# Kernel tuning notes

Measured on AMD Instinct MI355X. Metric: run time of the kernel, lower is better.

## Reference

```python
import jax, jax.numpy as jnp
import numpy as np

TIME_STEP = 32
BATCH = 1048576


def setup_inputs() -> dict:
    key = jax.random.key(0)
    k_x, k_w, k_b = jax.random.split(key, 3)
    inputs = jax.random.normal(k_x, (BATCH, TIME_STEP), dtype=jnp.float32)
    # Row t of W holds the weights of nn.Linear(t+1, 1); entries j>t are unused (masked).
    # Match torch Linear init scale: U(-1/sqrt(fan_in), 1/sqrt(fan_in)) per row, roughly -> just use small uniform.
    W = jax.random.uniform(k_w, (TIME_STEP, TIME_STEP), dtype=jnp.float32, minval=-0.5, maxval=0.5)
    b = jax.random.uniform(k_b, (TIME_STEP,), dtype=jnp.float32, minval=-0.5, maxval=0.5)
    return {"inputs": inputs, "W": W, "b": b}


def reference(inputs, W, b):
    # out[n, t] = sum_{j <= t} W[t, j] * inputs[n, j] + b[t]
    # Fuse the T tiny linears into one triangular-masked matmul.
    Wtri = jnp.tril(W)                       # [T, T] lower triangular
    return jnp.einsum("nj,tj->nt", inputs, Wtri) + b  # [B, T]
```

## Files before the change

### kernel.cpp

```cpp
#include <hip/hip_runtime.h>


constexpr int T    = 32;
constexpr int ROWS = 256;

__global__ __launch_bounds__(256) void triu_kernel(
    const float* __restrict__ x, const float* __restrict__ W,
    const float* __restrict__ b, float* __restrict__ out)
{
    __shared__ float4 sX[ROWS * 8];

    const int tid  = threadIdx.x;
    const int lane = tid & 63;
    const int wid  = tid >> 6;
    const long long base4 = (long long)blockIdx.x * (ROWS * 8);

    const float4* __restrict__ x4 = reinterpret_cast<const float4*>(x) + base4;

    #pragma unroll
    for (int it = 0; it < 8; ++it) {
        const int s   = it * 256 + wid * 64 + lane;
        const int row = s >> 3;
        const int c   = (s & 7) ^ (row & 7);
        __builtin_amdgcn_global_load_lds(
            (const __attribute__((address_space(1))) void*)(x4 + row * 8 + c),
            (__attribute__((address_space(3))) void*)(&sX[it * 256 + wid * 64]),
            16, 0, 0);
    }
    __syncthreads();

    const int r7 = tid & 7;
    float xr[T];
    #pragma unroll
    for (int k = 0; k < 8; ++k) {
        const float4 v = sX[tid * 8 + (k ^ r7)];
        xr[4 * k + 0] = v.x; xr[4 * k + 1] = v.y;
        xr[4 * k + 2] = v.z; xr[4 * k + 3] = v.w;
    }

    float acc[T];
    #pragma unroll
    for (int t = 0; t < T; ++t) {
        float a = b[t];
        #pragma unroll
        for (int j = 0; j <= t; ++j)
            a = fmaf(W[t * T + j], xr[j], a);
        acc[t] = a;
    }

    #pragma unroll
    for (int k = 0; k < 8; ++k)
        sX[tid * 8 + (k ^ r7)] = make_float4(acc[4 * k + 0], acc[4 * k + 1],
                                             acc[4 * k + 2], acc[4 * k + 3]);
    __syncthreads();

    float4* __restrict__ o4 = reinterpret_cast<float4*>(out) + base4;
    #pragma unroll
    for (int it = 0; it < 8; ++it) {
        const int idx = it * 256 + tid;
        const int row = idx >> 3;
        o4[idx] = sX[row * 8 + ((idx & 7) ^ (row & 7))];
    }
}

extern "C" void kernel_launch(void* const* d_in, const int* in_sizes, int n_in,
                              void* d_out, int out_size, void* d_ws, size_t ws_size,
                              hipStream_t stream) {
    const float* x  = (const float*)d_in[0];
    const float* W  = (const float*)d_in[1];
    const float* b  = (const float*)d_in[2];
    float* out      = (float*)d_out;

    const int batch = in_sizes[0] / T;
    const int grid  = batch / ROWS;
    triu_kernel<<<grid, 256, 0, stream>>>(x, W, b, out);
}
```

Baseline: 243.5 us.

## Make blocks persistent over several tiles with double-buffered async LDS loads

Each block now handles eight 256-row tiles instead of one. While the current tile is computed and stored, the next tile is prefetched into a second LDS buffer with global_load_lds. Manual vmcnt/lgkmcnt waits and s_barrier calls sequence the buffers, and the grid shrinks by the tile factor. This aims to hide load latency and cut launch/block overhead. In exchange, doubling LDS per block with a grid of only a few blocks per CU lowers occupancy and memory-level parallelism.

```diff
diff --git a/kernel.cpp b/kernel.cpp
--- a/kernel.cpp
+++ b/kernel.cpp
@@ -1,66 +1,88 @@
 #include <hip/hip_runtime.h>
 
 
-constexpr int T    = 32;
-constexpr int ROWS = 256;
+constexpr int T         = 32;
+constexpr int ROWS      = 256;
+constexpr int TPB_TILES = 8;
 
 __global__ __launch_bounds__(256) void triu_kernel(
     const float* __restrict__ x, const float* __restrict__ W,
     const float* __restrict__ b, float* __restrict__ out)
 {
-    __shared__ float4 sX[ROWS * 8];
+    __shared__ float4 sX[2][ROWS * 8];
 
     const int tid  = threadIdx.x;
     const int lane = tid & 63;
     const int wid  = tid >> 6;
-    const long long base4 = (long long)blockIdx.x * (ROWS * 8);
+    const int r7   = tid & 7;
 
-    const float4* __restrict__ x4 = reinterpret_cast<const float4*>(x) + base4;
+    const float4* __restrict__ x4 = reinterpret_cast<const float4*>(x);
+    float4*       __restrict__ o4 = reinterpret_cast<float4*>(out);
 
-    #pragma unroll
-    for (int it = 0; it < 8; ++it) {
-        const int s   = it * 256 + wid * 64 + lane;
-        const int row = s >> 3;
-        const int c   = (s & 7) ^ (row & 7);
-        __builtin_amdgcn_global_load_lds(
-            (const __attribute__((address_space(1))) void*)(x4 + row * 8 + c),
-            (__attribute__((address_space(3))) void*)(&sX[it * 256 + wid * 64]),
-            16, 0, 0);
+    const long long tile0 = (long long)blockIdx.x * TPB_TILES;
+
+    const int lrow = lane >> 3;
+    const int lsrc = wid * 64 + lrow * 8 + ((lane & 7) ^ lrow);
+
+    #define STAGE(g, buf)                                                     \
+        do {                                                                  \
+            const float4* _src = x4 + (tile0 + (g)) * (ROWS * 8) + lsrc;      \
+            _Pragma("unroll")                                                 \
+            for (int it = 0; it < 8; ++it) {                                  \
+                __builtin_amdgcn_global_load_lds(                             \
+                    (const __attribute__((address_space(1))) void*)(_src + it * 256), \
+                    (__attribute__((address_space(3))) void*)(&sX[(buf)][it * 256 + wid * 64]), \
+                    16, 0, 0);                                                \
+            }                                                                 \
+        } while (0)
+
+    STAGE(0, 0);
+
+    for (int i = 0; i < TPB_TILES; ++i) {
+        const int cur = i & 1;
+
+        if (i == 0) { asm volatile("s_waitcnt vmcnt(0)" ::: "memory"); }
+        else        { asm volatile("s_waitcnt vmcnt(8)" ::: "memory"); }
+        __builtin_amdgcn_sched_barrier(0);
+        __builtin_amdgcn_s_barrier();
+
+        if (i + 1 < TPB_TILES) STAGE(i + 1, cur ^ 1);
+
+        float xr[T];
+        #pragma unroll
+        for (int k = 0; k < 8; ++k) {
+            const float4 v = sX[cur][tid * 8 + (k ^ r7)];
+            xr[4*k+0] = v.x; xr[4*k+1] = v.y; xr[4*k+2] = v.z; xr[4*k+3] = v.w;
+        }
+
+        float acc[T];
+        #pragma unroll
+        for (int t = 0; t < T; ++t) {
+            float a = b[t];
+            #pragma unroll
+            for (int j = 0; j <= t; ++j)
+                a = fmaf(W[t * T + j], xr[j], a);
+            acc[t] = a;
+        }
+
+        #pragma unroll
+        for (int k = 0; k < 8; ++k)
+            sX[cur][tid * 8 + (k ^ r7)] =
+                make_float4(acc[4*k+0], acc[4*k+1], acc[4*k+2], acc[4*k+3]);
+
+        asm volatile("s_waitcnt lgkmcnt(0)" ::: "memory");
+        __builtin_amdgcn_sched_barrier(0);
+        __builtin_amdgcn_s_barrier();
+
+        float4* dst = o4 + (tile0 + i) * (ROWS * 8);
+        #pragma unroll
+        for (int it = 0; it < 8; ++it) {
+            const int idx = it * 256 + tid;
+            const int row = idx >> 3;
+            dst[idx] = sX[cur][row * 8 + ((idx & 7) ^ (row & 7))];
+        }
     }
-    __syncthreads();
-
-    const int r7 = tid & 7;
-    float xr[T];
-    #pragma unroll
-    for (int k = 0; k < 8; ++k) {
-        const float4 v = sX[tid * 8 + (k ^ r7)];
-        xr[4 * k + 0] = v.x; xr[4 * k + 1] = v.y;
-        xr[4 * k + 2] = v.z; xr[4 * k + 3] = v.w;
-    }
-
-    float acc[T];
-    #pragma unroll
-    for (int t = 0; t < T; ++t) {
-        float a = b[t];
-        #pragma unroll
-        for (int j = 0; j <= t; ++j)
-            a = fmaf(W[t * T + j], xr[j], a);
-        acc[t] = a;
-    }
-
-    #pragma unroll
-    for (int k = 0; k < 8; ++k)
-        sX[tid * 8 + (k ^ r7)] = make_float4(acc[4 * k + 0], acc[4 * k + 1],
-                                             acc[4 * k + 2], acc[4 * k + 3]);
-    __syncthreads();
-
-    float4* __restrict__ o4 = reinterpret_cast<float4*>(out) + base4;
-    #pragma unroll
-    for (int it = 0; it < 8; ++it) {
-        const int idx = it * 256 + tid;
-        const int row = idx >> 3;
-        o4[idx] = sX[row * 8 + ((idx & 7) ^ (row & 7))];
-    }
+    #undef STAGE
 }
 
 extern "C" void kernel_launch(void* const* d_in, const int* in_sizes, int n_in,
@@ -72,6 +94,6 @@
     float* out      = (float*)d_out;
 
     const int batch = in_sizes[0] / T;
-    const int grid  = batch / ROWS;
+    const int grid  = batch / (ROWS * TPB_TILES);
     triu_kernel<<<grid, 256, 0, stream>>>(x, W, b, out);
 }
```

Result: slower. 252.7 us (+3.8%).
